# Optimization experiments

Hardware: AMD Instinct MI355X
Metric: run time of the kernel (lower is better)

The kernel has to match this reference:

```python
import jax, jax.numpy as jnp
import numpy as np

B, N = 2, 8192
FUN, EMB = 7, 3
H = 512
HEADS = 8
DH = H // HEADS  # 64
G = 32           # slice_num
L = 4            # n_layers
OUT = 4
MLP_H = 4 * H


def _ln(x, g, b, eps=1e-5):
    m = x.mean(-1, keepdims=True)
    v = ((x - m) ** 2).mean(-1, keepdims=True)
    return (x - m) * jax.lax.rsqrt(v + eps) * g + b


def _forward(fun, emb, W_pre1, b_pre1, W_pre2, b_pre2, placeholder,
             ln1_g, ln1_b, Wfx, bfx, Wx, bx, Wslice, bslice, temp,
             Wq, Wk, Wv, Wo, bo, ln2_g, ln2_b, Wm1, bm1, Wm2, bm2,
             lnf_g, lnf_b, Wout, bout):
    b, n = fun.shape[0], fun.shape[1]
    gelu = lambda z: jax.nn.gelu(z, approximate=False)  # torch nn.GELU default (erf)
    # preprocess MLP (n_layers=0, res=False): act(pre(x)) -> post
    x = jnp.concatenate([emb, fun], axis=-1)            # [B,N,EMB+FUN]
    fx = gelu(x @ W_pre1 + b_pre1) @ W_pre2 + b_pre2    # [B,N,H]
    fx = fx + placeholder
    scale = DH ** -0.5
    for l in range(L):
        # --- physics attention (irregular mesh) ---
        h = _ln(fx, ln1_g[l], ln1_b[l])
        fx_mid = (h @ Wfx[l] + bfx[l]).reshape(b, n, HEADS, DH)  # bnhd
        x_mid = (h @ Wx[l] + bx[l]).reshape(b, n, HEADS, DH)
        logits = jnp.einsum('bnhd,dg->bnhg', x_mid, Wslice[l]) + bslice[l]
        sw = jax.nn.softmax(logits / temp[l][None, None, :, None], axis=-1)  # bnhg
        slice_mass = sw.sum(axis=1)                                   # bhg
        token = jnp.einsum('bnhd,bnhg->bhgd', fx_mid, sw)
        token = token / (slice_mass[..., None] + 1e-5)                # bhgd
        q = token @ Wq[l]
        k = token @ Wk[l]
        v = token @ Wv[l]
        attn = jax.nn.softmax(jnp.einsum('bhgd,bhkd->bhgk', q, k) * scale, axis=-1)
        out_tok = jnp.einsum('bhgk,bhkd->bhgd', attn, v)
        out = jnp.einsum('bhgd,bnhg->bnhd', out_tok, sw).reshape(b, n, H)
        fx = out @ Wo[l] + bo[l] + fx
        # --- LN + MLP (hidden = 4H) with residual ---
        h2 = _ln(fx, ln2_g[l], ln2_b[l])
        fx = gelu(h2 @ Wm1[l] + bm1[l]) @ Wm2[l] + bm2[l] + fx
    # last-layer head: LN -> Linear(out_dim)
    return _ln(fx, lnf_g, lnf_b) @ Wout + bout


def setup_inputs() -> dict:
    key = jax.random.key(0)
    ks = iter(jax.random.split(key, 64))
    nrm = lambda shape, s=0.02: jax.random.normal(next(ks), shape, jnp.float32) * s
    return dict(
        fun=jax.random.normal(next(ks), (B, N, FUN), jnp.float32),
        emb=jax.random.normal(next(ks), (B, N, EMB), jnp.float32),
        W_pre1=nrm((FUN + EMB, 2 * H)), b_pre1=jnp.zeros((2 * H,), jnp.float32),
        W_pre2=nrm((2 * H, H)), b_pre2=jnp.zeros((H,), jnp.float32),
        placeholder=nrm((H,), 1.0),
        ln1_g=jnp.ones((L, H), jnp.float32), ln1_b=jnp.zeros((L, H), jnp.float32),
        Wfx=nrm((L, H, H)), bfx=jnp.zeros((L, H), jnp.float32),
        Wx=nrm((L, H, H)), bx=jnp.zeros((L, H), jnp.float32),
        Wslice=nrm((L, DH, G), 0.1), bslice=jnp.zeros((L, G), jnp.float32),
        temp=jnp.full((L, HEADS), 0.5, jnp.float32),
        Wq=nrm((L, DH, DH)), Wk=nrm((L, DH, DH)), Wv=nrm((L, DH, DH)),
        Wo=nrm((L, H, H)), bo=jnp.zeros((L, H), jnp.float32),
        ln2_g=jnp.ones((L, H), jnp.float32), ln2_b=jnp.zeros((L, H), jnp.float32),
        Wm1=nrm((L, H, MLP_H)), bm1=jnp.zeros((L, MLP_H), jnp.float32),
        Wm2=nrm((L, MLP_H, H)), bm2=jnp.zeros((L, H), jnp.float32),
        lnf_g=jnp.ones((H,), jnp.float32), lnf_b=jnp.zeros((H,), jnp.float32),
        Wout=nrm((H, OUT)), bout=jnp.zeros((OUT,), jnp.float32),
    )


def reference(fun, emb, W_pre1, b_pre1, W_pre2, b_pre2, placeholder,
              ln1_g, ln1_b, Wfx, bfx, Wx, bx, Wslice, bslice, temp,
              Wq, Wk, Wv, Wo, bo, ln2_g, ln2_b, Wm1, bm1, Wm2, bm2,
              lnf_g, lnf_b, Wout, bout):
    return _forward(fun, emb, W_pre1, b_pre1, W_pre2, b_pre2, placeholder,
                    ln1_g, ln1_b, Wfx, bfx, Wx, bx, Wslice, bslice, temp,
                    Wq, Wk, Wv, Wo, bo, ln2_g, ln2_b, Wm1, bm1, Wm2, bm2,
                    lnf_g, lnf_b, Wout, bout)
```

## Files before the change

### kernel.cpp

```cpp
#include <hip/hip_runtime.h>
#include <hip/hip_bf16.h>
#include <cstdint>
#include <cstddef>

typedef float  f32x4  __attribute__((ext_vector_type(4)));
typedef __bf16 bf16x8 __attribute__((ext_vector_type(8)));
typedef __bf16 bf16x4 __attribute__((ext_vector_type(4)));

#define DEV __device__ __forceinline__

DEV float gelu_f(float x){ return 0.5f * x * (1.0f + erff(x * 0.70710678118654752f)); }

DEV void gl16(void* lds, const void* g){
  __builtin_amdgcn_global_load_lds((const __attribute__((address_space(1))) void*)g,
                                   (__attribute__((address_space(3))) void*)lds, 16, 0, 0);
}

static constexpr size_t OFF_FX     = 0;
static constexpr size_t OFF_H      = 33554432;
static constexpr size_t OFF_REGA   = 50331648;
static constexpr size_t OFF_FXMID  = OFF_REGA;
static constexpr size_t OFF_SW     = OFF_REGA + 16777216;
static constexpr size_t OFF_MLPH   = OFF_REGA;
static constexpr size_t OFF_H1     = OFF_REGA;
static constexpr size_t OFF_OUTB   = OFF_REGA + 67108864;
static constexpr size_t OFF_PT     = OFF_OUTB + 16777216;
static constexpr size_t OFF_PTM    = OFF_PT + 2097152;
static constexpr size_t OFF_OT     = OFF_PTM + 32768;
static constexpr size_t OFF_WT     = OFF_OT + 131072;
static constexpr size_t OFF_BIAS   = OFF_WT + 23068672;

__global__ __launch_bounds__(256) void wtrans_k(const float* __restrict__ W, __bf16* __restrict__ Wt,
                                                int K, int N, size_t wstride, size_t wtstride)
{
  __shared__ float tile[64][65];
  W  += (size_t)blockIdx.z * wstride;
  Wt += (size_t)blockIdx.z * wtstride;
  int t = threadIdx.x;
  int k0 = blockIdx.x * 64, n0 = blockIdx.y * 64;
  #pragma unroll
  for (int i = 0; i < 16; i++){
    int e = t + 256*i; int kk = e >> 6, nn = e & 63;
    tile[kk][nn] = W[(size_t)(k0+kk)*N + n0+nn];
  }
  __syncthreads();
  #pragma unroll
  for (int i = 0; i < 16; i++){
    int e = t + 256*i; int nn = e >> 6, kk = e & 63;
    Wt[(size_t)(n0+nn)*K + k0+kk] = (__bf16)tile[kk][nn];
  }
}

__global__ __launch_bounds__(128) void prep_wxs_k(const float* __restrict__ Wx, const float* __restrict__ Wsl,
                                                  const float* __restrict__ bx, const float* __restrict__ bsl,
                                                  const float* __restrict__ temp,
                                                  __bf16* __restrict__ Btcat, float* __restrict__ bcat)
{
  __shared__ float wsc[64];
  int l = blockIdx.y;
  const float* Wx_l  = Wx  + (size_t)l*262144;
  const float* Wsl_l = Wsl + l*2048;
  const float* bx_l  = bx  + l*512;
  const float* bsl_l = bsl + l*32;
  __bf16* Wt_l = Btcat + (size_t)l*393216 + (size_t)512*512;
  float* blog_l = bcat + l*768 + 512;
  int hg = blockIdx.x; int h = hg >> 5, g = hg & 31;
  int t = threadIdx.x;
  if (t < 64) wsc[t] = Wsl_l[t*32 + g];
  __syncthreads();
  float invt = 1.0f / temp[l*8 + h];
  #pragma unroll
  for (int cc = 0; cc < 4; cc++){
    int c = t + cc*128;
    float a = 0.f;
    for (int d = 0; d < 64; d++) a += Wx_l[(size_t)c*512 + h*64 + d] * wsc[d];
    Wt_l[(size_t)hg*512 + c] = (__bf16)(a * invt);
  }
  if (t == 0){
    float a = 0.f;
    for (int d = 0; d < 64; d++) a += bx_l[h*64 + d] * wsc[d];
    blog_l[hg] = (a + bsl_l[g]) * invt;
  }
}

__global__ __launch_bounds__(256) void bias_setup_k(const float* __restrict__ b_pre2, const float* __restrict__ placeholder,
                                                    const float* __restrict__ bfx,
                                                    float* __restrict__ bpre2p, float* __restrict__ bcat)
{
  int i = blockIdx.x*256 + threadIdx.x;
  if (i < 512) bpre2p[i] = b_pre2[i] + placeholder[i];
  else if (i < 2560){
    int j = i - 512; int l = j >> 9, c = j & 511;
    bcat[l*768 + c] = bfx[l*512 + c];
  }
}

__global__ __launch_bounds__(256) void preproc1_k(const float* __restrict__ fun, const float* __restrict__ emb,
                                                  const float* __restrict__ W1, const float* __restrict__ b1,
                                                  __bf16* __restrict__ h1)
{
  __shared__ float w1l[10][1024];
  int t = threadIdx.x;
  for (int i = t*4; i < 10240; i += 1024) *(f32x4*)&w1l[0][i] = *(const f32x4*)&W1[i];
  __syncthreads();
  f32x4 bv = *(const f32x4*)&b1[t*4];
  int r0 = blockIdx.x * 4;
  for (int r = 0; r < 4; r++){
    int m = r0 + r;
    const float* er = emb + (size_t)m*3;
    const float* fr = fun + (size_t)m*7;
    float x[10];
    x[0]=er[0]; x[1]=er[1]; x[2]=er[2];
    #pragma unroll
    for (int c = 0; c < 7; c++) x[3+c] = fr[c];
    f32x4 acc = bv;
    #pragma unroll
    for (int c = 0; c < 10; c++){
      f32x4 wv = *(const f32x4*)&w1l[c][t*4];
      acc += x[c] * wv;
    }
    __bf16* op = h1 + (size_t)m*1024 + t*4;
    #pragma unroll
    for (int e = 0; e < 4; e++) op[e] = (__bf16)gelu_f(acc[e]);
  }
}

template<int EPI, int BN>
__global__ __launch_bounds__(512) void gemm_wide(const __bf16* __restrict__ A, const __bf16* __restrict__ Bt,
                                                 const float* __restrict__ bias, const float* __restrict__ res,
                                                 void* __restrict__ outp, void* __restrict__ outp2,
                                                 int N, int lgK)
{
  constexpr int NSUB_B = BN/16;
  constexpr int S = 16 + NSUB_B;
  constexpr int Q = S/8;
  constexpr int NJ = BN/32;
  __shared__ bf16x8 ldsAB[3][S][64];
  const int tid = threadIdx.x;
  const int w = tid >> 6, lane = tid & 63;
  const int lm = lane & 15, lq = lane >> 4;
  const int wr = w >> 1, wc = w & 1;
  const int m0 = blockIdx.x * 256, n0 = blockIdx.y * BN;
  const int niter = 1 << (lgK - 5);

  auto issue = [&](int i){
    unsigned buf = (unsigned)i % 3u;
    int kk = i << 5;
    #pragma unroll
    for (int q = 0; q < Q; q++){
      int f = w*Q + q;
      const __bf16* p = (f < 16)
        ? A  + (((size_t)(m0 + f*16 + lm)) << lgK) + kk + lq*8
        : Bt + (((size_t)(n0 + (f-16)*16 + lm)) << lgK) + kk + lq*8;
      gl16(&ldsAB[buf][f][0], p);
    }
  };

  issue(0); issue(1);

  f32x4 acc[4][NJ] = {};

  for (int i = 0; i < niter; ++i){
    if (i + 2 < niter){
      issue(i + 2);
      if constexpr (Q == 4) __builtin_amdgcn_s_waitcnt(0x0F78);
      else                  __builtin_amdgcn_s_waitcnt(0x0F76);
    } else if (i + 1 < niter){
      if constexpr (Q == 4) __builtin_amdgcn_s_waitcnt(0x0F74);
      else                  __builtin_amdgcn_s_waitcnt(0x0F73);
    } else {
      __builtin_amdgcn_s_waitcnt(0x0F70);
    }
    __builtin_amdgcn_s_barrier();
    const unsigned buf = (unsigned)i % 3u;
    bf16x8 af[4], bfr[NJ];
    #pragma unroll
    for (int ii = 0; ii < 4; ii++)  af[ii]  = ldsAB[buf][wr*4 + ii][lane];
    #pragma unroll
    for (int jj = 0; jj < NJ; jj++) bfr[jj] = ldsAB[buf][16 + wc*NJ + jj][lane];
    #pragma unroll
    for (int ii = 0; ii < 4; ii++)
      #pragma unroll
      for (int jj = 0; jj < NJ; jj++)
        acc[ii][jj] = __builtin_amdgcn_mfma_f32_16x16x32_bf16(af[ii], bfr[jj], acc[ii][jj], 0, 0, 0);
    __builtin_amdgcn_s_barrier();
  }

  if (EPI == 4 && blockIdx.y == 2){
    float* swp = (float*)outp2;
    #pragma unroll
    for (int ii = 0; ii < 4; ii++){
      int row0 = m0 + wr*64 + ii*16 + lq*4;
      #pragma unroll
      for (int hp = 0; hp < 4; hp++){
        int j0 = hp*2, j1 = j0 + 1;
        int h = wc*4 + hp;
        float b0 = bias[512 + wc*128 + j0*16 + lm];
        float b1 = bias[512 + wc*128 + j1*16 + lm];
        #pragma unroll
        for (int r = 0; r < 4; r++){
          int row = row0 + r;
          float v0 = acc[ii][j0][r] + b0;
          float v1 = acc[ii][j1][r] + b1;
          float mx = fmaxf(v0, v1);
          #pragma unroll
          for (int msk = 8; msk; msk >>= 1) mx = fmaxf(mx, __shfl_xor(mx, msk));
          float e0 = expf(v0 - mx), e1 = expf(v1 - mx);
          float ss = e0 + e1;
          #pragma unroll
          for (int msk = 8; msk; msk >>= 1) ss += __shfl_xor(ss, msk);
          float inv = 1.f / ss;
          int b = row >> 13, n = row & 8191;
          float* op = swp + ((size_t)(b*8 + h)*8192 + n)*32;
          op[lm]      = e0 * inv;
          op[16 + lm] = e1 * inv;
        }
      }
    }
    return;
  }

  #pragma unroll
  for (int ii = 0; ii < 4; ii++){
    int row0 = m0 + wr*64 + ii*16 + lq*4;
    #pragma unroll
    for (int jj = 0; jj < NJ; jj++){
      int col = n0 + wc*(BN/2) + jj*16 + lm;
      float bv = bias[col];
      #pragma unroll
      for (int r = 0; r < 4; r++){
        size_t idx = (size_t)(row0 + r)*N + col;
        float v = acc[ii][jj][r] + bv;
        if (EPI == 2) v += res[idx];
        if (EPI == 1)      ((__bf16*)outp)[idx] = (__bf16)gelu_f(v);
        else if (EPI == 4) ((__bf16*)outp)[idx] = (__bf16)v;
        else               ((float*)outp)[idx]  = v;
      }
    }
  }
}

__global__ __launch_bounds__(256) void ln_k(const float* __restrict__ x, const float* __restrict__ g,
                                            const float* __restrict__ b, __bf16* __restrict__ out)
{
  int w = threadIdx.x >> 6, lane = threadIdx.x & 63;
  int row = blockIdx.x*4 + w;
  const float* xr = x + (size_t)row*512 + lane*8;
  float v[8];
  *(f32x4*)&v[0] = *(const f32x4*)xr;
  *(f32x4*)&v[4] = *(const f32x4*)(xr + 4);
  float s = 0.f, sq = 0.f;
  #pragma unroll
  for (int e = 0; e < 8; e++){ s += v[e]; sq += v[e]*v[e]; }
  #pragma unroll
  for (int off = 32; off; off >>= 1){ s += __shfl_xor(s, off); sq += __shfl_xor(sq, off); }
  float mean = s * (1.f/512.f);
  float var  = sq * (1.f/512.f) - mean*mean;
  float rstd = rsqrtf(var + 1e-5f);
  float gv[8], bv[8];
  *(f32x4*)&gv[0] = *(const f32x4*)(g + lane*8);
  *(f32x4*)&gv[4] = *(const f32x4*)(g + lane*8 + 4);
  *(f32x4*)&bv[0] = *(const f32x4*)(b + lane*8);
  *(f32x4*)&bv[4] = *(const f32x4*)(b + lane*8 + 4);
  __bf16* op = out + (size_t)row*512 + lane*8;
  #pragma unroll
  for (int e = 0; e < 8; e++) op[e] = (__bf16)((v[e]-mean)*rstd*gv[e] + bv[e]);
}

__global__ __launch_bounds__(256) void token_part_k(const __bf16* __restrict__ fxmid, const float* __restrict__ sw,
                                                    float* __restrict__ pt, float* __restrict__ ptm)
{
  __shared__ float fxl[32][64];
  __shared__ float swl[32][32];
  int t = threadIdx.x;
  int chunk = blockIdx.x, bh = blockIdx.y;
  int b = bh >> 3, h = bh & 7;
  int d = t & 63, gg = (t >> 6) * 8;
  float acc[8] = {0,0,0,0,0,0,0,0};
  float macc = 0.f;
  for (int s = 0; s < 16; s++){
    int nbase = chunk*512 + s*32;
    __syncthreads();
    #pragma unroll
    for (int i = 0; i < 2; i++){
      int e = t + 256*i; int rv = e >> 4, c4 = e & 15;
      bf16x4 v = *(const bf16x4*)&fxmid[((size_t)(b*8192 + nbase + rv))*512 + h*64 + c4*4];
      fxl[rv][c4*4+0] = (float)v[0];
      fxl[rv][c4*4+1] = (float)v[1];
      fxl[rv][c4*4+2] = (float)v[2];
      fxl[rv][c4*4+3] = (float)v[3];
    }
    { int rv = t >> 3, c4 = t & 7;
      *(f32x4*)&swl[rv][c4*4] = *(const f32x4*)&sw[((size_t)bh*8192 + nbase + rv)*32 + c4*4]; }
    __syncthreads();
    for (int nn = 0; nn < 32; nn++){
      float f = fxl[nn][d];
      #pragma unroll
      for (int jj = 0; jj < 8; jj++) acc[jj] += f * swl[nn][gg+jj];
    }
    if (t < 32){ for (int nn = 0; nn < 32; nn++) macc += swl[nn][t]; }
  }
  int cb = chunk*16 + bh;
  #pragma unroll
  for (int jj = 0; jj < 8; jj++)
    pt[((size_t)cb*32 + gg + jj)*64 + d] = acc[jj];
  if (t < 32) ptm[cb*32 + t] = macc;
}

__global__ __launch_bounds__(256) void attn_k(const float* __restrict__ pt, const float* __restrict__ ptm,
                                              const float* __restrict__ Wq, const float* __restrict__ Wk,
                                              const float* __restrict__ Wv, float* __restrict__ ot)
{
  __shared__ float tok[32][64];
  __shared__ float ml[32];
  __shared__ float qq[32][65], kk2[32][65], vv[32][65];
  __shared__ float at[32][33];
  int t = threadIdx.x, bh = blockIdx.x;
  if (t < 32){
    float s = 0.f;
    for (int c = 0; c < 16; c++) s += ptm[(c*16 + bh)*32 + t];
    ml[t] = s + 1e-5f;
  }
  __syncthreads();
  #pragma unroll
  for (int i = 0; i < 8; i++){
    int e = t + 256*i; int g = e >> 6, d = e & 63;
    float s = 0.f;
    for (int c = 0; c < 16; c++) s += pt[((size_t)(c*16 + bh)*32 + g)*64 + d];
    tok[g][d] = s / ml[g];
  }
  __syncthreads();
  #pragma unroll
  for (int i = 0; i < 8; i++){
    int e = t + 256*i; int g = e >> 6, j = e & 63;
    float aq = 0.f, ak = 0.f, av = 0.f;
    for (int d = 0; d < 64; d++){
      float tv = tok[g][d];
      aq += tv * Wq[d*64 + j];
      ak += tv * Wk[d*64 + j];
      av += tv * Wv[d*64 + j];
    }
    qq[g][j] = aq; kk2[g][j] = ak; vv[g][j] = av;
  }
  __syncthreads();
  #pragma unroll
  for (int i = 0; i < 4; i++){
    int e = t + 256*i; int g = e >> 5, j2 = e & 31;
    float s2 = 0.f;
    for (int d = 0; d < 64; d++) s2 += qq[g][d] * kk2[j2][d];
    at[g][j2] = s2 * 0.125f;
  }
  __syncthreads();
  if (t < 32){
    float mx = at[t][0];
    for (int j = 1; j < 32; j++) mx = fmaxf(mx, at[t][j]);
    float ss = 0.f;
    for (int j = 0; j < 32; j++){ float e2 = expf(at[t][j]-mx); at[t][j] = e2; ss += e2; }
    float inv = 1.f / ss;
    for (int j = 0; j < 32; j++) at[t][j] *= inv;
  }
  __syncthreads();
  #pragma unroll
  for (int i = 0; i < 8; i++){
    int e = t + 256*i; int g = e >> 6, d = e & 63;
    float s3 = 0.f;
    for (int j = 0; j < 32; j++) s3 += at[g][j] * vv[j][d];
    ot[(size_t)bh*2048 + e] = s3;
  }
}

__global__ __launch_bounds__(256) void deslice_k(const float* __restrict__ ot, const float* __restrict__ sw,
                                                 __bf16* __restrict__ outb)
{
  __shared__ float otl[32][64];
  __shared__ float swl[128][36];
  int t = threadIdx.x;
  int chunk = blockIdx.x, bh = blockIdx.y;
  int b = bh >> 3, h = bh & 7;
  int n0 = chunk*128;
  #pragma unroll
  for (int i = 0; i < 8; i++){
    int e = t + 256*i;
    otl[e>>6][e&63] = ot[(size_t)bh*2048 + e];
  }
  {
    int r = t >> 1, half = t & 1;
    const float* sp = sw + ((size_t)bh*8192 + n0 + r)*32 + half*16;
    float* dp = &swl[r][half*16];
    #pragma unroll
    for (int q = 0; q < 4; q++) *(f32x4*)(dp + q*4) = *(const f32x4*)(sp + q*4);
  }
  __syncthreads();
  const int nl = t >> 4;
  const int d0 = (t & 15) * 4;
  float o[8][4] = {};
  for (int g = 0; g < 32; g++){
    f32x4 ov = *(const f32x4*)&otl[g][d0];
    #pragma unroll
    for (int p = 0; p < 8; p++){
      float s = swl[p*16 + nl][g];
      o[p][0] += s * ov[0]; o[p][1] += s * ov[1];
      o[p][2] += s * ov[2]; o[p][3] += s * ov[3];
    }
  }
  #pragma unroll
  for (int p = 0; p < 8; p++){
    int n = n0 + p*16 + nl;
    bf16x4 v;
    v[0] = (__bf16)o[p][0]; v[1] = (__bf16)o[p][1];
    v[2] = (__bf16)o[p][2]; v[3] = (__bf16)o[p][3];
    *(bf16x4*)&outb[((size_t)(b*8192 + n))*512 + h*64 + d0] = v;
  }
}

__global__ __launch_bounds__(256) void head_k(const float* __restrict__ x, const float* __restrict__ g,
                                              const float* __restrict__ b, const float* __restrict__ Wout,
                                              const float* __restrict__ bout, float* __restrict__ out)
{
  int w = threadIdx.x >> 6, lane = threadIdx.x & 63;
  int row = blockIdx.x*4 + w;
  const float* xr = x + (size_t)row*512 + lane*8;
  float v[8];
  *(f32x4*)&v[0] = *(const f32x4*)xr;
  *(f32x4*)&v[4] = *(const f32x4*)(xr + 4);
  float s = 0.f, sq = 0.f;
  #pragma unroll
  for (int e = 0; e < 8; e++){ s += v[e]; sq += v[e]*v[e]; }
  #pragma unroll
  for (int off = 32; off; off >>= 1){ s += __shfl_xor(s, off); sq += __shfl_xor(sq, off); }
  float mean = s * (1.f/512.f);
  float rstd = rsqrtf(sq * (1.f/512.f) - mean*mean + 1e-5f);
  float o[4] = {0,0,0,0};
  #pragma unroll
  for (int e = 0; e < 8; e++){
    int c = lane*8 + e;
    float yn = (v[e]-mean)*rstd*g[c] + b[c];
    const float* wr = Wout + (size_t)c*4;
    o[0] += yn*wr[0]; o[1] += yn*wr[1]; o[2] += yn*wr[2]; o[3] += yn*wr[3];
  }
  #pragma unroll
  for (int off = 32; off; off >>= 1){
    #pragma unroll
    for (int j = 0; j < 4; j++) o[j] += __shfl_xor(o[j], off);
  }
  if (lane == 0){
    #pragma unroll
    for (int j = 0; j < 4; j++) out[(size_t)row*4 + j] = o[j] + bout[j];
  }
}

extern "C" void kernel_launch(void* const* d_in, const int* in_sizes, int n_in,
                              void* d_out, int out_size, void* d_ws, size_t ws_size,
                              hipStream_t stream)
{
  const float* fun    = (const float*)d_in[0];
  const float* emb    = (const float*)d_in[1];
  const float* W_pre1 = (const float*)d_in[2];
  const float* b_pre1 = (const float*)d_in[3];
  const float* W_pre2 = (const float*)d_in[4];
  const float* b_pre2 = (const float*)d_in[5];
  const float* placeholder = (const float*)d_in[6];
  const float* ln1_g  = (const float*)d_in[7];
  const float* ln1_b  = (const float*)d_in[8];
  const float* Wfx    = (const float*)d_in[9];
  const float* bfx    = (const float*)d_in[10];
  const float* Wx     = (const float*)d_in[11];
  const float* bx     = (const float*)d_in[12];
  const float* Wslice = (const float*)d_in[13];
  const float* bslice = (const float*)d_in[14];
  const float* temp   = (const float*)d_in[15];
  const float* Wq     = (const float*)d_in[16];
  const float* Wk     = (const float*)d_in[17];
  const float* Wv     = (const float*)d_in[18];
  const float* Wo     = (const float*)d_in[19];
  const float* bo     = (const float*)d_in[20];
  const float* ln2_g  = (const float*)d_in[21];
  const float* ln2_b  = (const float*)d_in[22];
  const float* Wm1    = (const float*)d_in[23];
  const float* bm1    = (const float*)d_in[24];
  const float* Wm2    = (const float*)d_in[25];
  const float* bm2    = (const float*)d_in[26];
  const float* lnf_g  = (const float*)d_in[27];
  const float* lnf_b  = (const float*)d_in[28];
  const float* Wout   = (const float*)d_in[29];
  const float* bout   = (const float*)d_in[30];

  char* ws = (char*)d_ws;
  float*  fx     = (float*)(ws + OFF_FX);
  __bf16* hbf    = (__bf16*)(ws + OFF_H);
  __bf16* fxmid  = (__bf16*)(ws + OFF_FXMID);
  float*  sw     = (float*)(ws + OFF_SW);
  __bf16* mlph   = (__bf16*)(ws + OFF_MLPH);
  __bf16* h1bf   = (__bf16*)(ws + OFF_H1);
  __bf16* outb   = (__bf16*)(ws + OFF_OUTB);
  float*  pt     = (float*)(ws + OFF_PT);
  float*  ptm    = (float*)(ws + OFF_PTM);
  float*  ot     = (float*)(ws + OFF_OT);
  __bf16* Wpre2t = (__bf16*)(ws + OFF_WT);
  __bf16* Btcat  = (__bf16*)(ws + OFF_WT + 1048576);
  __bf16* Wot    = (__bf16*)(ws + OFF_WT + 4194304);
  __bf16* Wm1t   = (__bf16*)(ws + OFF_WT + 6291456);
  __bf16* Wm2t   = (__bf16*)(ws + OFF_WT + 14680064);
  float*  bcat   = (float*)(ws + OFF_BIAS);
  float*  bpre2p = (float*)(ws + OFF_BIAS + 4*768*4);

  wtrans_k<<<dim3(16,8,1), 256,0,stream>>>(W_pre2, Wpre2t, 1024, 512, 0, 0);
  wtrans_k<<<dim3(8,8,4),  256,0,stream>>>(Wfx, Btcat, 512, 512, 262144, 393216);
  wtrans_k<<<dim3(8,8,4),  256,0,stream>>>(Wo,  Wot,  512, 512, 262144, 262144);
  wtrans_k<<<dim3(8,32,4), 256,0,stream>>>(Wm1, Wm1t, 512, 2048, 1048576, 1048576);
  wtrans_k<<<dim3(32,8,4), 256,0,stream>>>(Wm2, Wm2t, 2048, 512, 1048576, 1048576);
  prep_wxs_k<<<dim3(256,4),128,0,stream>>>(Wx, Wslice, bx, bslice, temp, Btcat, bcat);
  bias_setup_k<<<10,256,0,stream>>>(b_pre2, placeholder, bfx, bpre2p, bcat);

  preproc1_k<<<4096,256,0,stream>>>(fun, emb, W_pre1, b_pre1, h1bf);
  gemm_wide<0,128><<<dim3(64,4),512,0,stream>>>(h1bf, Wpre2t, bpre2p, nullptr, (void*)fx, nullptr, 512, 10);

  for (int l = 0; l < 4; l++){
    ln_k<<<4096,256,0,stream>>>(fx, ln1_g + l*512, ln1_b + l*512, hbf);
    gemm_wide<4,256><<<dim3(64,3),512,0,stream>>>(hbf, Btcat + (size_t)l*393216, bcat + l*768, nullptr, (void*)fxmid, (void*)sw, 512, 9);
    token_part_k<<<dim3(16,16),256,0,stream>>>(fxmid, sw, pt, ptm);
    attn_k<<<16,256,0,stream>>>(pt, ptm, Wq + l*4096, Wk + l*4096, Wv + l*4096, ot);
    deslice_k<<<dim3(64,16),256,0,stream>>>(ot, sw, outb);
    gemm_wide<2,128><<<dim3(64,4),512,0,stream>>>(outb, Wot + (size_t)l*262144, bo + l*512, fx, (void*)fx, nullptr, 512, 9);
    ln_k<<<4096,256,0,stream>>>(fx, ln2_g + l*512, ln2_b + l*512, hbf);
    gemm_wide<1,256><<<dim3(64,8),512,0,stream>>>(hbf, Wm1t + (size_t)l*1048576, bm1 + l*2048, nullptr, (void*)mlph, nullptr, 2048, 9);
    gemm_wide<2,128><<<dim3(64,4),512,0,stream>>>(mlph, Wm2t + (size_t)l*1048576, bm2 + l*512, fx, (void*)fx, nullptr, 512, 11);
  }

  head_k<<<4096,256,0,stream>>>(fx, lnf_g, lnf_b, Wout, bout, (float*)d_out);
}
```

Baseline: 1.341 ms.

## Replace direct global-to-LDS triple buffering with register-staged double buffering in GEMM

The wide GEMM previously used global_load_lds DMA into a three-stage LDS ring with vmcnt waits. It now loads the next K-slice into registers, writes the current one into a two-stage LDS buffer, and uses one barrier pair per iteration. The aim is to cut LDS footprint (possibly raising occupancy) and simplify synchronisation. In exchange it adds VGPR pressure and an extra register-to-LDS store per iteration, and global-load latency is hidden by only one slice of prefetch.

```diff
diff --git a/kernel.cpp b/kernel.cpp
--- a/kernel.cpp
+++ b/kernel.cpp
@@ -11,10 +11,7 @@
 
 DEV float gelu_f(float x){ return 0.5f * x * (1.0f + erff(x * 0.70710678118654752f)); }
 
-DEV void gl16(void* lds, const void* g){
-  __builtin_amdgcn_global_load_lds((const __attribute__((address_space(1))) void*)g,
-                                   (__attribute__((address_space(3))) void*)lds, 16, 0, 0);
-}
+#define WAIT_LGKM0 0xC07F
 
 static constexpr size_t OFF_FX     = 0;
 static constexpr size_t OFF_H      = 33554432;
@@ -135,7 +132,7 @@
   constexpr int S = 16 + NSUB_B;
   constexpr int Q = S/8;
   constexpr int NJ = BN/32;
-  __shared__ bf16x8 ldsAB[3][S][64];
+  __shared__ bf16x8 ldsAB[2][S][64];
   const int tid = threadIdx.x;
   const int w = tid >> 6, lane = tid & 63;
   const int lm = lane & 15, lq = lane >> 4;
@@ -143,36 +140,33 @@
   const int m0 = blockIdx.x * 256, n0 = blockIdx.y * BN;
   const int niter = 1 << (lgK - 5);
 
-  auto issue = [&](int i){
-    unsigned buf = (unsigned)i % 3u;
-    int kk = i << 5;
-    #pragma unroll
-    for (int q = 0; q < Q; q++){
-      int f = w*Q + q;
-      const __bf16* p = (f < 16)
-        ? A  + (((size_t)(m0 + f*16 + lm)) << lgK) + kk + lq*8
-        : Bt + (((size_t)(n0 + (f-16)*16 + lm)) << lgK) + kk + lq*8;
-      gl16(&ldsAB[buf][f][0], p);
-    }
-  };
-
-  issue(0); issue(1);
+  const __bf16* gp[Q];
+  #pragma unroll
+  for (int q = 0; q < Q; q++){
+    int f = w*Q + q;
+    gp[q] = (f < 16)
+      ? A  + (((size_t)(m0 + f*16 + lm)) << lgK) + lq*8
+      : Bt + (((size_t)(n0 + (f-16)*16 + lm)) << lgK) + lq*8;
+  }
+
+  bf16x8 r[Q];
+  #pragma unroll
+  for (int q = 0; q < Q; q++){ r[q] = *(const bf16x8*)gp[q]; gp[q] += 32; }
 
   f32x4 acc[4][NJ] = {};
 
   for (int i = 0; i < niter; ++i){
-    if (i + 2 < niter){
-      issue(i + 2);
-      if constexpr (Q == 4) __builtin_amdgcn_s_waitcnt(0x0F78);
-      else                  __builtin_amdgcn_s_waitcnt(0x0F76);
-    } else if (i + 1 < niter){
-      if constexpr (Q == 4) __builtin_amdgcn_s_waitcnt(0x0F74);
-      else                  __builtin_amdgcn_s_waitcnt(0x0F73);
-    } else {
-      __builtin_amdgcn_s_waitcnt(0x0F70);
-    }
     __builtin_amdgcn_s_barrier();
-    const unsigned buf = (unsigned)i % 3u;
+    const unsigned buf = (unsigned)i & 1u;
+    #pragma unroll
+    for (int q = 0; q < Q; q++)
+      ldsAB[buf][w*Q + q][lane] = r[q];
+    if (i + 1 < niter){
+      #pragma unroll
+      for (int q = 0; q < Q; q++){ r[q] = *(const bf16x8*)gp[q]; gp[q] += 32; }
+    }
+    __builtin_amdgcn_s_waitcnt(WAIT_LGKM0);
+    __builtin_amdgcn_s_barrier();
     bf16x8 af[4], bfr[NJ];
     #pragma unroll
     for (int ii = 0; ii < 4; ii++)  af[ii]  = ldsAB[buf][wr*4 + ii][lane];
@@ -183,7 +177,6 @@
       #pragma unroll
       for (int jj = 0; jj < NJ; jj++)
         acc[ii][jj] = __builtin_amdgcn_mfma_f32_16x16x32_bf16(af[ii], bfr[jj], acc[ii][jj], 0, 0, 0);
-    __builtin_amdgcn_s_barrier();
   }
 
   if (EPI == 4 && blockIdx.y == 2){
@@ -198,10 +191,10 @@
         float b0 = bias[512 + wc*128 + j0*16 + lm];
         float b1 = bias[512 + wc*128 + j1*16 + lm];
         #pragma unroll
-        for (int r = 0; r < 4; r++){
-          int row = row0 + r;
-          float v0 = acc[ii][j0][r] + b0;
-          float v1 = acc[ii][j1][r] + b1;
+        for (int r2 = 0; r2 < 4; r2++){
+          int row = row0 + r2;
+          float v0 = acc[ii][j0][r2] + b0;
+          float v1 = acc[ii][j1][r2] + b1;
           float mx = fmaxf(v0, v1);
           #pragma unroll
           for (int msk = 8; msk; msk >>= 1) mx = fmaxf(mx, __shfl_xor(mx, msk));
@@ -228,9 +221,9 @@
       int col = n0 + wc*(BN/2) + jj*16 + lm;
       float bv = bias[col];
       #pragma unroll
-      for (int r = 0; r < 4; r++){
-        size_t idx = (size_t)(row0 + r)*N + col;
-        float v = acc[ii][jj][r] + bv;
+      for (int r2 = 0; r2 < 4; r2++){
+        size_t idx = (size_t)(row0 + r2)*N + col;
+        float v = acc[ii][jj][r2] + bv;
         if (EPI == 2) v += res[idx];
         if (EPI == 1)      ((__bf16*)outp)[idx] = (__bf16)gelu_f(v);
         else if (EPI == 4) ((__bf16*)outp)[idx] = (__bf16)v;
```

Result: no change. 1.334 ms (-0.5%).
